# Kernel optimization log

Hardware: AMD Instinct MI355X
Metric: run time of the kernel (lower is better)

The kernel has to match this reference:

```python
import jax, jax.numpy as jnp
import numpy as np

DEG20 = 20.0 * np.pi / 180.0
MIN_PATCH_AREA = 4.0


def _bilinear(p, sy, sx):
    """Bilinear sample [P,P,3] patch at float coords sy,sx of shape [H,W]."""
    P = p.shape[0]
    y0 = jnp.floor(sy)
    x0 = jnp.floor(sx)
    wy = (sy - y0)[..., None]
    wx = (sx - x0)[..., None]
    y0i = jnp.clip(y0, 0, P - 1).astype(jnp.int32)
    y1i = jnp.clip(y0 + 1, 0, P - 1).astype(jnp.int32)
    x0i = jnp.clip(x0, 0, P - 1).astype(jnp.int32)
    x1i = jnp.clip(x0 + 1, 0, P - 1).astype(jnp.int32)
    v00 = p[y0i, x0i]
    v01 = p[y0i, x1i]
    v10 = p[y1i, x0i]
    v11 = p[y1i, x1i]
    return v00 * (1 - wy) * (1 - wx) + v01 * (1 - wy) * wx + v10 * wy * (1 - wx) + v11 * wy * wx


def setup_inputs() -> dict:
    key = jax.random.key(0)
    B, H, W, N, P = 16, 768, 768, 16, 640
    k_img, k_patch, k_ymin, k_xmin, k_h, k_w = jax.random.split(key, 6)
    images = jax.random.uniform(k_img, (B, H, W, 3), jnp.float32, -1.0, 1.0)
    patch = jax.random.uniform(k_patch, (P, P, 3), jnp.float32, -1.0, 1.0)
    ymin = jax.random.uniform(k_ymin, (B, N), jnp.float32, 0.0, 0.55 * H)
    xmin = jax.random.uniform(k_xmin, (B, N), jnp.float32, 0.0, 0.55 * W)
    bh = jax.random.uniform(k_h, (B, N), jnp.float32, 60.0, 0.40 * H)
    bw = jax.random.uniform(k_w, (B, N), jnp.float32, 60.0, 0.40 * W)
    ymax = jnp.minimum(ymin + bh, float(H))
    xmax = jnp.minimum(xmin + bw, float(W))
    boxes = jnp.stack([ymin, xmin, ymax, xmax], axis=-1)  # [B,N,4]
    scale = jnp.float32(0.4)
    return {"images": images, "boxes": boxes, "patch": patch, "scale": scale}


def reference(images, boxes, patch, scale):
    B, H, W, _ = images.shape
    P = patch.shape[0]
    Hf, Wf = jnp.float32(H), jnp.float32(W)
    yy = jnp.arange(H, dtype=jnp.float32)[:, None]  # [H,1]
    xx = jnp.arange(W, dtype=jnp.float32)[None, :]  # [1,W]
    scale_s = jnp.reshape(scale, ())

    def per_image(img, bxs, ikey):
        kw, kb, kboxes = jax.random.split(ikey, 3)
        # random_print_adjust: w*patch + b, clipped
        wmul = 0.5 + 0.1 * jax.random.normal(kw, (1, 1, 3), jnp.float32)
        badd = 0.01 * jax.random.normal(kb, (1, 1, 3), jnp.float32)
        p = jnp.clip(wmul * patch + badd, -1.0, 1.0)
        # brightness matcher: shift patch mean toward image mean
        p = jnp.clip(p + (jnp.mean(img) - jnp.mean(p)), -1.0, 1.0)
        bkeys = jax.random.split(kboxes, bxs.shape[0])

        def step(im, inp):
            box, bk = inp
            k1, k2, k3, k4, k5 = jax.random.split(bk, 5)
            ymin, xmin, ymax, xmax = box[0], box[1], box[2], box[3]
            bh = ymax - ymin
            bw = xmax - xmin
            longer = jnp.maximum(bh, bw)
            psize = jnp.floor(longer * scale_s)            # patch_h == patch_w
            diag = jnp.minimum(jnp.float32(np.sqrt(2.0)) * psize, Wf)
            tol = 0.2
            oy = ymin + bh / 2 + jax.random.uniform(k1, (), jnp.float32, -tol * bh / 2, tol * bh / 2)
            ox = xmin + bw / 2 + jax.random.uniform(k2, (), jnp.float32, -tol * bw / 2, tol * bw / 2)
            y0 = jnp.maximum(oy - diag / 2, 0.0)
            x0 = jnp.maximum(ox - diag / 2, 0.0)
            y0 = jnp.where(y0 + diag > Hf, Hf - diag, y0)
            x0 = jnp.where(x0 + diag > Wf, Wf - diag, x0)
            # TF casts to int32 (truncation; values >= 0 -> floor)
            y0 = jnp.floor(y0)
            x0 = jnp.floor(x0)
            d = jnp.floor(diag)
            ph = psize
            valid = (ph * ph) > MIN_PATCH_AREA
            top = jnp.floor((d - ph) / 2.0)                # pad offset
            angle = jax.random.uniform(k3, (), jnp.float32, -DEG20, DEG20)
            # pixel coords inside the diag x diag patch window
            u = yy - y0                                    # [H,1] -> broadcast [H,W]
            v = xx - x0
            inside = (u >= 0) & (u < d) & (v >= 0) & (v < d)
            c = (d - 1.0) / 2.0
            ca, sa = jnp.cos(angle), jnp.sin(angle)
            iu = c + ca * (u - c) - sa * (v - c)           # inverse rotation about center
            iv = c + sa * (u - c) + ca * (v - c)
            py = iu - top                                  # coords in resized patch
            px = iv - top
            # bilinear resize (half-pixel centers): src = (dst+0.5)*P/ph - 0.5
            sy = (py + 0.5) * (P / ph) - 0.5
            sx = (px + 0.5) * (P / ph) - 0.5
            val = _bilinear(p, sy, sx)                     # [H,W,3]
            noise = jax.random.uniform(k4, (H, W, 3), jnp.float32, -0.01, 0.01)
            delta = jax.random.uniform(k5, (), jnp.float32, -0.3, 0.3)
            val = jnp.clip(val + noise + delta, -1.0, 1.0)
            in_patch = (py >= 0) & (py <= ph - 1) & (px >= 0) & (px <= ph - 1)
            fill = jnp.where(in_patch[..., None], val, -2.0)  # pad/rotate fill = -2
            blended = jnp.clip(jnp.where(fill < -1.0, im, fill), -1.0, 1.0)
            write = inside[..., None] & valid
            return jnp.where(write, blended, im), None

        out, _ = jax.lax.scan(step, img, (bxs, bkeys))
        return out

    ikeys = jax.random.split(jax.random.key(42), B)
    return jax.vmap(per_image)(images, boxes, ikeys)
```

## Files before the change

kernel.cpp:

```cpp
#include <hip/hip_runtime.h>
#include <stdint.h>

#define NIMG 16
#define IMH 768
#define IMW 768
#define NBOX 16
#define PSZ 640
#define IMG_ELEMS (IMH*IMW*3)
#define PATCH_ELEMS (PSZ*PSZ*3)
#define CPBLK 128
#define PATBLK 64
#define PADBLK 64
#define RENDER_BLKS 4096

typedef float f4 __attribute__((ext_vector_type(4)));

__device__ __forceinline__ uint32_t rotl32(uint32_t v, int r){ return (v<<r)|(v>>(32-r)); }

__device__ __forceinline__ void threefry(uint32_t k0, uint32_t k1, uint32_t c0, uint32_t c1,
                                         uint32_t& o0, uint32_t& o1){
  uint32_t ks2 = k0 ^ k1 ^ 0x1BD11BDAu;
  uint32_t x0 = c0 + k0, x1 = c1 + k1;
#define TFR(r) { x0 += x1; x1 = rotl32(x1,(r)); x1 ^= x0; }
  TFR(13) TFR(15) TFR(26) TFR(6)
  x0 += k1;  x1 += ks2 + 1u;
  TFR(17) TFR(29) TFR(16) TFR(24)
  x0 += ks2; x1 += k0 + 2u;
  TFR(13) TFR(15) TFR(26) TFR(6)
  x0 += k0;  x1 += k1 + 3u;
  TFR(17) TFR(29) TFR(16) TFR(24)
  x0 += k1;  x1 += ks2 + 4u;
  TFR(13) TFR(15) TFR(26) TFR(6)
  x0 += ks2; x1 += k0 + 5u;
#undef TFR
  o0 = x0; o1 = x1;
}

__device__ __forceinline__ uint32_t rbits(uint32_t k0, uint32_t k1, uint32_t idx){
  uint32_t a, b; threefry(k0, k1, 0u, idx, a, b); return a ^ b;
}

__device__ __forceinline__ float u01(uint32_t bits){
  return __uint_as_float((bits >> 9) | 0x3f800000u) - 1.0f;
}

__device__ __forceinline__ float juniform(uint32_t k0, uint32_t k1, uint32_t idx, float mn, float mx){
  float u = u01(rbits(k0, k1, idx));
  float span = __fsub_rn(mx, mn);
  return fmaxf(mn, __fadd_rn(__fmul_rn(u, span), mn));
}

__device__ float erfinv32(float x){
  float w = -log1pf(-x*x);
  float p;
  if (w < 5.0f){
    w = w - 2.5f;
    p = 2.81022636e-08f;
    p = fmaf(p,w, 3.43273939e-07f);
    p = fmaf(p,w,-3.5233877e-06f);
    p = fmaf(p,w,-4.39150654e-06f);
    p = fmaf(p,w, 0.00021858087f);
    p = fmaf(p,w,-0.00125372503f);
    p = fmaf(p,w,-0.00417768164f);
    p = fmaf(p,w, 0.246640727f);
    p = fmaf(p,w, 1.50140941f);
  } else {
    w = sqrtf(w) - 3.0f;
    p = -0.000200214257f;
    p = fmaf(p,w, 0.000100950558f);
    p = fmaf(p,w, 0.00134934322f);
    p = fmaf(p,w,-0.00367342844f);
    p = fmaf(p,w, 0.00573950773f);
    p = fmaf(p,w,-0.0076224613f);
    p = fmaf(p,w, 0.00943887047f);
    p = fmaf(p,w, 1.00167406f);
    p = fmaf(p,w, 2.83297682f);
  }
  return p * x;
}

__device__ __forceinline__ void compute_wb(int b, float* rec){
  uint32_t i0,i1; threefry(0u, 42u, 0u, (uint32_t)b, i0, i1);
  uint32_t kw0,kw1; threefry(i0, i1, 0u, 0u, kw0, kw1);
  uint32_t kb0,kb1; threefry(i0, i1, 0u, 1u, kb0, kb1);
  const float lo = -0.99999994f;
  const float span = __fsub_rn(1.0f, lo);
  const float sq2 = 1.4142135623730951f;
  for (int j = 0; j < 3; j++){
    float uw = u01(rbits(kw0, kw1, (uint32_t)j));
    float rw = fmaxf(lo, __fadd_rn(__fmul_rn(uw, span), lo));
    float nw = __fmul_rn(sq2, erfinv32(rw));
    rec[j] = __fadd_rn(0.5f, __fmul_rn(0.1f, nw));
    float ub = u01(rbits(kb0, kb1, (uint32_t)j));
    float rb = fmaxf(lo, __fadd_rn(__fmul_rn(ub, span), lo));
    float nb = __fmul_rn(sq2, erfinv32(rb));
    rec[3+j] = __fmul_rn(0.01f, nb);
  }
  rec[6] = 0.0f; rec[7] = 0.0f;
}

__global__ __launch_bounds__(256) void k_front(const float* __restrict__ img,
                                               const float* __restrict__ patch,
                                               float* __restrict__ out,
                                               double* __restrict__ imgpart,
                                               double* __restrict__ patpart,
                                               f4* __restrict__ pad4, int do_pad){
  if (blockIdx.x < PATBLK){
    __shared__ float wl[NIMG*8];
    if (threadIdx.x < NIMG) compute_wb(threadIdx.x, &wl[threadIdx.x*8]);
    __syncthreads();
    double s[NIMG];
    #pragma unroll
    for (int im = 0; im < NIMG; im++) s[im] = 0.0;
    const f4* p4 = (const f4*)patch;
    const int N4 = PATCH_ELEMS/4;
    for (int i = blockIdx.x*256 + threadIdx.x; i < N4; i += PATBLK*256){
      f4 v = p4[i];
      int c = (i << 2) % 3;
      #pragma unroll
      for (int q = 0; q < 4; q++){
        float pv = v[q];
        #pragma unroll
        for (int im = 0; im < NIMG; im++){
          float t = __fadd_rn(__fmul_rn(wl[im*8 + c], pv), wl[im*8 + 3 + c]);
          t = fminf(fmaxf(t, -1.0f), 1.0f);
          s[im] += (double)t;
        }
        c = (c == 2) ? 0 : c + 1;
      }
    }
    #pragma unroll
    for (int im = 0; im < NIMG; im++)
      for (int o = 32; o > 0; o >>= 1) s[im] += __shfl_down(s[im], o);
    __shared__ double red[4][NIMG];
    if ((threadIdx.x & 63) == 0){
      int w = threadIdx.x >> 6;
      #pragma unroll
      for (int im = 0; im < NIMG; im++) red[w][im] = s[im];
    }
    __syncthreads();
    if (threadIdx.x < NIMG){
      double t = red[0][threadIdx.x] + red[1][threadIdx.x] + red[2][threadIdx.x] + red[3][threadIdx.x];
      patpart[threadIdx.x*PATBLK + blockIdx.x] = t;
    }
  } else if (blockIdx.x < PATBLK + NIMG*CPBLK){
    int bi = blockIdx.x - PATBLK;
    int b = bi >> 7;
    int j = bi & (CPBLK-1);
    const f4* src = (const f4*)(img + (size_t)b * IMG_ELEMS);
    f4* dst = (f4*)(out + (size_t)b * IMG_ELEMS);
    const int N4 = IMG_ELEMS/4;
    f4 fs = {0.0f, 0.0f, 0.0f, 0.0f};
    #pragma unroll 2
    for (int i = j*256 + threadIdx.x; i < N4; i += CPBLK*256){
      f4 v = src[i];
      dst[i] = v;
      fs += v;
    }
    double s = ((double)fs.x + (double)fs.y) + ((double)fs.z + (double)fs.w);
    for (int o = 32; o > 0; o >>= 1) s += __shfl_down(s, o);
    __shared__ double sm[4];
    if ((threadIdx.x & 63) == 0) sm[threadIdx.x >> 6] = s;
    __syncthreads();
    if (threadIdx.x == 0) imgpart[b*CPBLK + j] = sm[0]+sm[1]+sm[2]+sm[3];
  } else {
    if (!do_pad) return;
    int pb = blockIdx.x - (PATBLK + NIMG*CPBLK);
    const f4* src = (const f4*)patch;
    const int NG = PSZ*PSZ/4;
    for (int g = pb*256 + threadIdx.x; g < NG; g += PADBLK*256){
      f4 a = src[g*3+0], b2 = src[g*3+1], c2 = src[g*3+2];
      f4 t0 = {a.x,  a.y,  a.z,  0.0f};
      f4 t1 = {a.w,  b2.x, b2.y, 0.0f};
      f4 t2 = {b2.z, b2.w, c2.x, 0.0f};
      f4 t3 = {c2.y, c2.z, c2.w, 0.0f};
      pad4[g*4+0] = t0; pad4[g*4+1] = t1; pad4[g*4+2] = t2; pad4[g*4+3] = t3;
    }
  }
}

__global__ __launch_bounds__(256) void k_final(const double* __restrict__ imgpart,
                        const double* __restrict__ patpart,
                        float* __restrict__ shift, float* __restrict__ wbg,
                        float* __restrict__ boxp, int* __restrict__ chunkoff,
                        const float* __restrict__ boxes, const float* __restrict__ scale){
  int t = threadIdx.x;
  {
    int im = t >> 4, l = t & 15;
    double si = 0.0, sp = 0.0;
    #pragma unroll
    for (int j = 0; j < CPBLK/16; j++) si += imgpart[im*CPBLK + l + j*16];
    #pragma unroll
    for (int j = 0; j < PATBLK/16; j++) sp += patpart[im*PATBLK + l + j*16];
    #pragma unroll
    for (int o = 8; o > 0; o >>= 1){ si += __shfl_down(si, o); sp += __shfl_down(sp, o); }
    if (l == 0){
      float mi = (float)(si / (double)IMG_ELEMS);
      float mp = (float)(sp / (double)PATCH_ELEMS);
      shift[im] = __fsub_rn(mi, mp);
      compute_wb(im, &wbg[im*8]);
    }
  }

  int nch = 0;
  {
    int b = t / NBOX, i = t % NBOX;
    uint32_t i0,i1;  threefry(0u, 42u, 0u, (uint32_t)b, i0, i1);
    uint32_t kx0,kx1; threefry(i0, i1, 0u, 2u, kx0, kx1);
    uint32_t bk0,bk1; threefry(kx0, kx1, 0u, (uint32_t)i, bk0, bk1);
    uint32_t K1a,K1b,K2a,K2b,K3a,K3b,K4a,K4b,K5a,K5b;
    threefry(bk0,bk1,0u,0u,K1a,K1b);
    threefry(bk0,bk1,0u,1u,K2a,K2b);
    threefry(bk0,bk1,0u,2u,K3a,K3b);
    threefry(bk0,bk1,0u,3u,K4a,K4b);
    threefry(bk0,bk1,0u,4u,K5a,K5b);

    const float* bx = boxes + (size_t)t*4;
    float ymin = bx[0], xmin = bx[1], ymax = bx[2], xmax = bx[3];
    float bh = __fsub_rn(ymax, ymin);
    float bw = __fsub_rn(xmax, xmin);
    float longer = fmaxf(bh, bw);
    float sc = scale[0];
    float psize = floorf(__fmul_rn(longer, sc));
    float diag = fminf(__fmul_rn(1.4142135623730951f, psize), 768.0f);

    float mny = __fdiv_rn(__fmul_rn(-0.2f, bh), 2.0f);
    float mxy = __fdiv_rn(__fmul_rn( 0.2f, bh), 2.0f);
    float r1 = juniform(K1a, K1b, 0u, mny, mxy);
    float oy = __fadd_rn(__fadd_rn(ymin, __fdiv_rn(bh, 2.0f)), r1);
    float mnx = __fdiv_rn(__fmul_rn(-0.2f, bw), 2.0f);
    float mxx = __fdiv_rn(__fmul_rn( 0.2f, bw), 2.0f);
    float r2 = juniform(K2a, K2b, 0u, mnx, mxx);
    float ox = __fadd_rn(__fadd_rn(xmin, __fdiv_rn(bw, 2.0f)), r2);

    float hd = __fdiv_rn(diag, 2.0f);
    float y0 = fmaxf(__fsub_rn(oy, hd), 0.0f);
    float x0 = fmaxf(__fsub_rn(ox, hd), 0.0f);
    if (__fadd_rn(y0, diag) > 768.0f) y0 = __fsub_rn(768.0f, diag);
    if (__fadd_rn(x0, diag) > 768.0f) x0 = __fsub_rn(768.0f, diag);
    y0 = floorf(y0);
    x0 = floorf(x0);
    float d  = floorf(diag);
    float ph = psize;
    float top = floorf(__fdiv_rn(__fsub_rn(d, ph), 2.0f));

    const float A20 = 0.3490658503988659f;
    float ang = juniform(K3a, K3b, 0u, -A20, A20);
    double da = (double)ang;
    float ca = (float)cos(da);
    float sa = (float)sin(da);
    float delta = juniform(K5a, K5b, 0u, -0.3f, 0.3f);
    float valid = (__fmul_rn(ph, ph) > 4.0f) ? 1.0f : 0.0f;
    float cc  = __fdiv_rn(__fsub_rn(d, 1.0f), 2.0f);
    float sres = __fdiv_rn(640.0f, ph);

    float* o = boxp + t*16;
    o[0]=y0; o[1]=x0; o[2]=d; o[3]=ph; o[4]=top; o[5]=cc; o[6]=ca; o[7]=sa;
    o[8]=sres; o[9]=delta;
    o[10]=__uint_as_float(K4a); o[11]=__uint_as_float(K4b);
    o[12]=valid; o[13]=__fsub_rn(ph, 1.0f); o[14]=0.0f; o[15]=0.0f;

    if (valid != 0.0f){
      int di = (int)d;
      nch = (di*di + 255) >> 8;
    }
  }

  __shared__ int scan[256];
  scan[t] = nch; __syncthreads();
  for (int off = 1; off < 256; off <<= 1){
    int v = (t >= off) ? scan[t-off] : 0;
    __syncthreads();
    scan[t] += v;
    __syncthreads();
  }
  if (t == 0) chunkoff[0] = 0;
  chunkoff[t+1] = scan[t];
}

template<int USEPAD>
__global__ __launch_bounds__(256) void k_render3(
    const float* __restrict__ patch, const f4* __restrict__ pad4,
    const float* __restrict__ wbg, const float* __restrict__ shiftg,
    const float* __restrict__ boxp, const int* __restrict__ chunkoff,
    float* __restrict__ out)
{
  __shared__ float sp[256*16];
  __shared__ float wl[NIMG*8];
  __shared__ float shl[NIMG];
  __shared__ int   coff[258];
  for (int i = threadIdx.x; i < 4096; i += 256) sp[i] = boxp[i];
  if (threadIdx.x < NIMG*8) wl[threadIdx.x] = wbg[threadIdx.x];
  if (threadIdx.x < NIMG)   shl[threadIdx.x] = shiftg[threadIdx.x];
  for (int i = threadIdx.x; i < 257; i += 256) coff[i] = chunkoff[i];
  __syncthreads();
  int total = coff[256];

  for (int chunk = blockIdx.x; chunk < total; chunk += RENDER_BLKS){
    int lo = 0, hi = 255;
    #pragma unroll
    for (int it = 0; it < 8; it++){
      int mid = (lo + hi + 1) >> 1;
      if (coff[mid] <= chunk) lo = mid; else hi = mid - 1;
    }
    int s = lo;
    const float* bp = &sp[s*16];
    int d = (int)bp[2];
    int dd = d*d;
    int idx = (chunk - coff[s])*256 + (int)threadIdx.x;
    if (idx >= dd) continue;

    int b = s >> 4, k = s & 15;
    float y0f = bp[0], x0f = bp[1];
    float cc = bp[5], ca = bp[6], sa = bp[7], top = bp[4];
    float ph1 = bp[13], sres = bp[8], delta = bp[9];

    int row = idx / d;
    int col = idx - row*d;
    int y = (int)y0f + row, x = (int)x0f + col;
    float yf = (float)y, xf = (float)x;
    float u = __fsub_rn(yf, y0f), v = __fsub_rn(xf, x0f);
    float um = __fsub_rn(u, cc), vm = __fsub_rn(v, cc);
    float iu = __fsub_rn(__fadd_rn(cc, __fmul_rn(ca, um)), __fmul_rn(sa, vm));
    float iv = __fadd_rn(__fadd_rn(cc, __fmul_rn(sa, um)), __fmul_rn(ca, vm));
    float py = __fsub_rn(iu, top), px = __fsub_rn(iv, top);
    if (!(py >= 0.0f && py <= ph1 && px >= 0.0f && px <= ph1)) continue;

    bool lose = false;
    for (int j = NBOX-1; j > k; --j){
      const float* bq = &sp[(b*NBOX + j)*16];
      if (bq[12] == 0.0f) continue;
      float u2 = __fsub_rn(yf, bq[0]);
      if (!(u2 >= 0.0f && u2 < bq[2])) continue;
      float v2 = __fsub_rn(xf, bq[1]);
      if (!(v2 >= 0.0f && v2 < bq[2])) continue;
      float um2 = __fsub_rn(u2, bq[5]), vm2 = __fsub_rn(v2, bq[5]);
      float iu2 = __fsub_rn(__fadd_rn(bq[5], __fmul_rn(bq[6], um2)), __fmul_rn(bq[7], vm2));
      float iv2 = __fadd_rn(__fadd_rn(bq[5], __fmul_rn(bq[7], um2)), __fmul_rn(bq[6], vm2));
      float py2 = __fsub_rn(iu2, bq[4]), px2 = __fsub_rn(iv2, bq[4]);
      if (py2 >= 0.0f && py2 <= bq[13] && px2 >= 0.0f && px2 <= bq[13]){ lose = true; break; }
    }
    if (lose) continue;

    float sy = __fsub_rn(__fmul_rn(__fadd_rn(py, 0.5f), sres), 0.5f);
    float sx = __fsub_rn(__fmul_rn(__fadd_rn(px, 0.5f), sres), 0.5f);
    float fy = floorf(sy), fx = floorf(sx);
    float wy = __fsub_rn(sy, fy), wx = __fsub_rn(sx, fx);
    int y0t = (int)fminf(fmaxf(fy, 0.0f), 639.0f);
    int y1t = (int)fminf(fmaxf(__fadd_rn(fy, 1.0f), 0.0f), 639.0f);
    int x0t = (int)fminf(fmaxf(fx, 0.0f), 639.0f);
    int x1t = (int)fminf(fmaxf(__fadd_rn(fx, 1.0f), 0.0f), 639.0f);
    float w00 = (1.0f-wy)*(1.0f-wx), w01 = (1.0f-wy)*wx;
    float w10 = wy*(1.0f-wx),        w11 = wy*wx;
    const float* wbb = &wl[b*8];
    float shf = shl[b];
    uint32_t n0 = __float_as_uint(bp[10]);
    uint32_t n1 = __float_as_uint(bp[11]);
    int pix = y*IMW + x;
    size_t base = (size_t)b*IMG_ELEMS + (size_t)pix*3;

    f4 p00, p01, p10, p11;
    int i00, i01, i10, i11;
    if constexpr (USEPAD){
      p00 = pad4[y0t*PSZ + x0t]; p01 = pad4[y0t*PSZ + x1t];
      p10 = pad4[y1t*PSZ + x0t]; p11 = pad4[y1t*PSZ + x1t];
      i00 = i01 = i10 = i11 = 0;
    } else {
      i00 = (y0t*PSZ + x0t)*3; i01 = (y0t*PSZ + x1t)*3;
      i10 = (y1t*PSZ + x0t)*3; i11 = (y1t*PSZ + x1t)*3;
    }
    #pragma unroll
    for (int c = 0; c < 3; c++){
      float wm = wbb[c], bd = wbb[3+c];
      float t00, t01, t10, t11;
      if constexpr (USEPAD){ t00 = p00[c]; t01 = p01[c]; t10 = p10[c]; t11 = p11[c]; }
      else { t00 = patch[i00+c]; t01 = patch[i01+c]; t10 = patch[i10+c]; t11 = patch[i11+c]; }
      float v00 = fminf(fmaxf(__fadd_rn(__fmul_rn(wm, t00), bd), -1.0f), 1.0f);
      v00 = fminf(fmaxf(__fadd_rn(v00, shf), -1.0f), 1.0f);
      float v01 = fminf(fmaxf(__fadd_rn(__fmul_rn(wm, t01), bd), -1.0f), 1.0f);
      v01 = fminf(fmaxf(__fadd_rn(v01, shf), -1.0f), 1.0f);
      float v10 = fminf(fmaxf(__fadd_rn(__fmul_rn(wm, t10), bd), -1.0f), 1.0f);
      v10 = fminf(fmaxf(__fadd_rn(v10, shf), -1.0f), 1.0f);
      float v11 = fminf(fmaxf(__fadd_rn(__fmul_rn(wm, t11), bd), -1.0f), 1.0f);
      v11 = fminf(fmaxf(__fadd_rn(v11, shf), -1.0f), 1.0f);
      float val = v00*w00 + v01*w01 + v10*w10 + v11*w11;
      float un = u01(rbits(n0, n1, (uint32_t)(pix*3 + c)));
      float span = __fsub_rn(0.01f, -0.01f);
      float nz = fmaxf(-0.01f, __fadd_rn(__fmul_rn(un, span), -0.01f));
      val = __fadd_rn(__fadd_rn(val, nz), delta);
      out[base + c] = fminf(fmaxf(val, -1.0f), 1.0f);
    }
  }
}

extern "C" void kernel_launch(void* const* d_in, const int* in_sizes, int n_in,
                              void* d_out, int out_size, void* d_ws, size_t ws_size,
                              hipStream_t stream){
  (void)in_sizes; (void)n_in; (void)out_size;
  const float* images = (const float*)d_in[0];
  const float* boxes  = (const float*)d_in[1];
  const float* patch  = (const float*)d_in[2];
  const float* scale  = (const float*)d_in[3];
  float* out = (float*)d_out;

  char* ws = (char*)d_ws;
  double* imgpart = (double*)(ws);
  double* patpart = (double*)(ws + 16384);
  float*  wb      = (float*)(ws + 24576);
  float*  shift   = (float*)(ws + 25088);
  float*  boxp    = (float*)(ws + 25600);
  int*    chunkoff= (int*)(ws + 41984);
  f4*     pad4    = (f4*)(ws + 65536);

  size_t need = 65536 + (size_t)PSZ*PSZ*16;
  int do_pad = (ws_size >= need) ? 1 : 0;

  int front_blks = PATBLK + NIMG*CPBLK + (do_pad ? PADBLK : 0);
  hipLaunchKernelGGL(k_front,   dim3(front_blks), dim3(256), 0, stream,
                     images, patch, out, imgpart, patpart, pad4, do_pad);
  hipLaunchKernelGGL(k_final,   dim3(1), dim3(256), 0, stream,
                     imgpart, patpart, shift, wb, boxp, chunkoff, boxes, scale);
  if (do_pad)
    hipLaunchKernelGGL(k_render3<1>, dim3(RENDER_BLKS), dim3(256), 0, stream,
                       patch, pad4, wb, shift, boxp, chunkoff, out);
  else
    hipLaunchKernelGGL(k_render3<0>, dim3(RENDER_BLKS), dim3(256), 0, stream,
                       patch, pad4, wb, shift, boxp, chunkoff, out);
}
```

Measured before the change: 139.1 us.

## Fuse image copy into per-pixel render pass using per-row box bitmasks

Drops the separate image copy from the front kernel; it now only computes the image sums. The render kernel now walks every output pixel: it loads the image values, checks per-row bitmasks of covering boxes built in k_final with shared-memory atomics, and composites the topmost patch that covers the pixel. Output is written with nontemporal stores. This removes the write-then-overwrite traffic and the chunk scan with its binary search, but the image is now read twice (once for the sums, once in render) and covered pixels loop over candidate boxes.

```diff
diff --git a/kernel.cpp b/kernel.cpp
--- a/kernel.cpp
+++ b/kernel.cpp
@@ -8,10 +8,10 @@
 #define PSZ 640
 #define IMG_ELEMS (IMH*IMW*3)
 #define PATCH_ELEMS (PSZ*PSZ*3)
-#define CPBLK 128
 #define PATBLK 64
 #define PADBLK 64
-#define RENDER_BLKS 4096
+#define ISUM 64
+#define RBLK_PER_IMG 576
 
 typedef float f4 __attribute__((ext_vector_type(4)));
 
@@ -101,7 +101,6 @@
 
 __global__ __launch_bounds__(256) void k_front(const float* __restrict__ img,
                                                const float* __restrict__ patch,
-                                               float* __restrict__ out,
                                                double* __restrict__ imgpart,
                                                double* __restrict__ patpart,
                                                f4* __restrict__ pad4, int do_pad){
@@ -143,29 +142,9 @@
       double t = red[0][threadIdx.x] + red[1][threadIdx.x] + red[2][threadIdx.x] + red[3][threadIdx.x];
       patpart[threadIdx.x*PATBLK + blockIdx.x] = t;
     }
-  } else if (blockIdx.x < PATBLK + NIMG*CPBLK){
-    int bi = blockIdx.x - PATBLK;
-    int b = bi >> 7;
-    int j = bi & (CPBLK-1);
-    const f4* src = (const f4*)(img + (size_t)b * IMG_ELEMS);
-    f4* dst = (f4*)(out + (size_t)b * IMG_ELEMS);
-    const int N4 = IMG_ELEMS/4;
-    f4 fs = {0.0f, 0.0f, 0.0f, 0.0f};
-    #pragma unroll 2
-    for (int i = j*256 + threadIdx.x; i < N4; i += CPBLK*256){
-      f4 v = src[i];
-      dst[i] = v;
-      fs += v;
-    }
-    double s = ((double)fs.x + (double)fs.y) + ((double)fs.z + (double)fs.w);
-    for (int o = 32; o > 0; o >>= 1) s += __shfl_down(s, o);
-    __shared__ double sm[4];
-    if ((threadIdx.x & 63) == 0) sm[threadIdx.x >> 6] = s;
-    __syncthreads();
-    if (threadIdx.x == 0) imgpart[b*CPBLK + j] = sm[0]+sm[1]+sm[2]+sm[3];
-  } else {
+  } else if (blockIdx.x < PATBLK + PADBLK){
     if (!do_pad) return;
-    int pb = blockIdx.x - (PATBLK + NIMG*CPBLK);
+    int pb = blockIdx.x - PATBLK;
     const f4* src = (const f4*)patch;
     const int NG = PSZ*PSZ/4;
     for (int g = pb*256 + threadIdx.x; g < NG; g += PADBLK*256){
@@ -176,20 +155,40 @@
       f4 t3 = {c2.y, c2.z, c2.w, 0.0f};
       pad4[g*4+0] = t0; pad4[g*4+1] = t1; pad4[g*4+2] = t2; pad4[g*4+3] = t3;
     }
+  } else {
+    int bi = blockIdx.x - (PATBLK + PADBLK);
+    int b = bi >> 6;
+    int j = bi & (ISUM-1);
+    const f4* src = (const f4*)(img + (size_t)b * IMG_ELEMS);
+    const int N4 = IMG_ELEMS/4;
+    f4 fs = {0.0f, 0.0f, 0.0f, 0.0f};
+    for (int i = j*256 + threadIdx.x; i < N4; i += ISUM*256){
+      f4 v = src[i];
+      fs += v;
+    }
+    double s = ((double)fs.x + (double)fs.y) + ((double)fs.z + (double)fs.w);
+    for (int o = 32; o > 0; o >>= 1) s += __shfl_down(s, o);
+    __shared__ double sm[4];
+    if ((threadIdx.x & 63) == 0) sm[threadIdx.x >> 6] = s;
+    __syncthreads();
+    if (threadIdx.x == 0) imgpart[b*ISUM + j] = sm[0]+sm[1]+sm[2]+sm[3];
   }
 }
 
 __global__ __launch_bounds__(256) void k_final(const double* __restrict__ imgpart,
                         const double* __restrict__ patpart,
                         float* __restrict__ shift, float* __restrict__ wbg,
-                        float* __restrict__ boxp, int* __restrict__ chunkoff,
+                        float* __restrict__ boxp, uint32_t* __restrict__ masks,
                         const float* __restrict__ boxes, const float* __restrict__ scale){
   int t = threadIdx.x;
+  __shared__ uint32_t rm[NIMG*IMH];
+  for (int i = t; i < NIMG*IMH; i += 256) rm[i] = 0u;
+
   {
     int im = t >> 4, l = t & 15;
     double si = 0.0, sp = 0.0;
     #pragma unroll
-    for (int j = 0; j < CPBLK/16; j++) si += imgpart[im*CPBLK + l + j*16];
+    for (int j = 0; j < ISUM/16; j++) si += imgpart[im*ISUM + l + j*16];
     #pragma unroll
     for (int j = 0; j < PATBLK/16; j++) sp += patpart[im*PATBLK + l + j*16];
     #pragma unroll
@@ -201,8 +200,8 @@
       compute_wb(im, &wbg[im*8]);
     }
   }
-
-  int nch = 0;
+  __syncthreads();
+
   {
     int b = t / NBOX, i = t % NBOX;
     uint32_t i0,i1;  threefry(0u, 42u, 0u, (uint32_t)b, i0, i1);
@@ -261,136 +260,125 @@
     o[12]=valid; o[13]=__fsub_rn(ph, 1.0f); o[14]=0.0f; o[15]=0.0f;
 
     if (valid != 0.0f){
-      int di = (int)d;
-      nch = (di*di + 255) >> 8;
-    }
-  }
-
-  __shared__ int scan[256];
-  scan[t] = nch; __syncthreads();
-  for (int off = 1; off < 256; off <<= 1){
-    int v = (t >= off) ? scan[t-off] : 0;
-    __syncthreads();
-    scan[t] += v;
-    __syncthreads();
-  }
-  if (t == 0) chunkoff[0] = 0;
-  chunkoff[t+1] = scan[t];
+      int y0i = (int)y0, di = (int)d;
+      uint32_t bit = 1u << i;
+      for (int y = y0i; y < y0i + di; y++)
+        atomicOr(&rm[b*IMH + y], bit);
+    }
+  }
+  __syncthreads();
+  for (int i = t; i < NIMG*IMH; i += 256) masks[i] = rm[i];
 }
 
 template<int USEPAD>
-__global__ __launch_bounds__(256) void k_render3(
-    const float* __restrict__ patch, const f4* __restrict__ pad4,
-    const float* __restrict__ wbg, const float* __restrict__ shiftg,
-    const float* __restrict__ boxp, const int* __restrict__ chunkoff,
-    float* __restrict__ out)
+__global__ __launch_bounds__(256) void k_render4(
+    const float* __restrict__ img, const float* __restrict__ patch,
+    const f4* __restrict__ pad4, const float* __restrict__ wbg,
+    const float* __restrict__ shiftg, const float* __restrict__ boxp,
+    const uint32_t* __restrict__ masks, float* __restrict__ out)
 {
-  __shared__ float sp[256*16];
-  __shared__ float wl[NIMG*8];
-  __shared__ float shl[NIMG];
-  __shared__ int   coff[258];
-  for (int i = threadIdx.x; i < 4096; i += 256) sp[i] = boxp[i];
-  if (threadIdx.x < NIMG*8) wl[threadIdx.x] = wbg[threadIdx.x];
-  if (threadIdx.x < NIMG)   shl[threadIdx.x] = shiftg[threadIdx.x];
-  for (int i = threadIdx.x; i < 257; i += 256) coff[i] = chunkoff[i];
+  int b   = blockIdx.x / RBLK_PER_IMG;
+  int blk = blockIdx.x - b*RBLK_PER_IMG;
+
+  __shared__ float sp[NBOX*16];
+  __shared__ float wl[8];
+  __shared__ float shl;
+  sp[threadIdx.x] = boxp[b*NBOX*16 + threadIdx.x];
+  if (threadIdx.x < 8) wl[threadIdx.x] = wbg[b*8 + threadIdx.x];
+  if (threadIdx.x == 0) shl = shiftg[b];
   __syncthreads();
-  int total = coff[256];
-
-  for (int chunk = blockIdx.x; chunk < total; chunk += RENDER_BLKS){
-    int lo = 0, hi = 255;
-    #pragma unroll
-    for (int it = 0; it < 8; it++){
-      int mid = (lo + hi + 1) >> 1;
-      if (coff[mid] <= chunk) lo = mid; else hi = mid - 1;
-    }
-    int s = lo;
-    const float* bp = &sp[s*16];
-    int d = (int)bp[2];
-    int dd = d*d;
-    int idx = (chunk - coff[s])*256 + (int)threadIdx.x;
-    if (idx >= dd) continue;
-
-    int b = s >> 4, k = s & 15;
-    float y0f = bp[0], x0f = bp[1];
-    float cc = bp[5], ca = bp[6], sa = bp[7], top = bp[4];
-    float ph1 = bp[13], sres = bp[8], delta = bp[9];
-
-    int row = idx / d;
-    int col = idx - row*d;
-    int y = (int)y0f + row, x = (int)x0f + col;
-    float yf = (float)y, xf = (float)x;
-    float u = __fsub_rn(yf, y0f), v = __fsub_rn(xf, x0f);
-    float um = __fsub_rn(u, cc), vm = __fsub_rn(v, cc);
-    float iu = __fsub_rn(__fadd_rn(cc, __fmul_rn(ca, um)), __fmul_rn(sa, vm));
-    float iv = __fadd_rn(__fadd_rn(cc, __fmul_rn(sa, um)), __fmul_rn(ca, vm));
-    float py = __fsub_rn(iu, top), px = __fsub_rn(iv, top);
-    if (!(py >= 0.0f && py <= ph1 && px >= 0.0f && px <= ph1)) continue;
-
-    bool lose = false;
-    for (int j = NBOX-1; j > k; --j){
-      const float* bq = &sp[(b*NBOX + j)*16];
-      if (bq[12] == 0.0f) continue;
-      float u2 = __fsub_rn(yf, bq[0]);
-      if (!(u2 >= 0.0f && u2 < bq[2])) continue;
-      float v2 = __fsub_rn(xf, bq[1]);
-      if (!(v2 >= 0.0f && v2 < bq[2])) continue;
-      float um2 = __fsub_rn(u2, bq[5]), vm2 = __fsub_rn(v2, bq[5]);
-      float iu2 = __fsub_rn(__fadd_rn(bq[5], __fmul_rn(bq[6], um2)), __fmul_rn(bq[7], vm2));
-      float iv2 = __fadd_rn(__fadd_rn(bq[5], __fmul_rn(bq[7], um2)), __fmul_rn(bq[6], vm2));
-      float py2 = __fsub_rn(iu2, bq[4]), px2 = __fsub_rn(iv2, bq[4]);
-      if (py2 >= 0.0f && py2 <= bq[13] && px2 >= 0.0f && px2 <= bq[13]){ lose = true; break; }
-    }
-    if (lose) continue;
-
-    float sy = __fsub_rn(__fmul_rn(__fadd_rn(py, 0.5f), sres), 0.5f);
-    float sx = __fsub_rn(__fmul_rn(__fadd_rn(px, 0.5f), sres), 0.5f);
-    float fy = floorf(sy), fx = floorf(sx);
-    float wy = __fsub_rn(sy, fy), wx = __fsub_rn(sx, fx);
-    int y0t = (int)fminf(fmaxf(fy, 0.0f), 639.0f);
-    int y1t = (int)fminf(fmaxf(__fadd_rn(fy, 1.0f), 0.0f), 639.0f);
-    int x0t = (int)fminf(fmaxf(fx, 0.0f), 639.0f);
-    int x1t = (int)fminf(fmaxf(__fadd_rn(fx, 1.0f), 0.0f), 639.0f);
-    float w00 = (1.0f-wy)*(1.0f-wx), w01 = (1.0f-wy)*wx;
-    float w10 = wy*(1.0f-wx),        w11 = wy*wx;
-    const float* wbb = &wl[b*8];
-    float shf = shl[b];
-    uint32_t n0 = __float_as_uint(bp[10]);
-    uint32_t n1 = __float_as_uint(bp[11]);
-    int pix = y*IMW + x;
-    size_t base = (size_t)b*IMG_ELEMS + (size_t)pix*3;
-
-    f4 p00, p01, p10, p11;
-    int i00, i01, i10, i11;
-    if constexpr (USEPAD){
-      p00 = pad4[y0t*PSZ + x0t]; p01 = pad4[y0t*PSZ + x1t];
-      p10 = pad4[y1t*PSZ + x0t]; p11 = pad4[y1t*PSZ + x1t];
-      i00 = i01 = i10 = i11 = 0;
-    } else {
-      i00 = (y0t*PSZ + x0t)*3; i01 = (y0t*PSZ + x1t)*3;
-      i10 = (y1t*PSZ + x0t)*3; i11 = (y1t*PSZ + x1t)*3;
-    }
-    #pragma unroll
-    for (int c = 0; c < 3; c++){
-      float wm = wbb[c], bd = wbb[3+c];
-      float t00, t01, t10, t11;
-      if constexpr (USEPAD){ t00 = p00[c]; t01 = p01[c]; t10 = p10[c]; t11 = p11[c]; }
-      else { t00 = patch[i00+c]; t01 = patch[i01+c]; t10 = patch[i10+c]; t11 = patch[i11+c]; }
-      float v00 = fminf(fmaxf(__fadd_rn(__fmul_rn(wm, t00), bd), -1.0f), 1.0f);
-      v00 = fminf(fmaxf(__fadd_rn(v00, shf), -1.0f), 1.0f);
-      float v01 = fminf(fmaxf(__fadd_rn(__fmul_rn(wm, t01), bd), -1.0f), 1.0f);
-      v01 = fminf(fmaxf(__fadd_rn(v01, shf), -1.0f), 1.0f);
-      float v10 = fminf(fmaxf(__fadd_rn(__fmul_rn(wm, t10), bd), -1.0f), 1.0f);
-      v10 = fminf(fmaxf(__fadd_rn(v10, shf), -1.0f), 1.0f);
-      float v11 = fminf(fmaxf(__fadd_rn(__fmul_rn(wm, t11), bd), -1.0f), 1.0f);
-      v11 = fminf(fmaxf(__fadd_rn(v11, shf), -1.0f), 1.0f);
-      float val = v00*w00 + v01*w01 + v10*w10 + v11*w11;
-      float un = u01(rbits(n0, n1, (uint32_t)(pix*3 + c)));
-      float span = __fsub_rn(0.01f, -0.01f);
-      float nz = fmaxf(-0.01f, __fadd_rn(__fmul_rn(un, span), -0.01f));
-      val = __fadd_rn(__fadd_rn(val, nz), delta);
-      out[base + c] = fminf(fmaxf(val, -1.0f), 1.0f);
-    }
-  }
+
+  int pixbase = blk*1024 + (int)threadIdx.x*4;
+  int y = pixbase / IMW;
+  int xb = pixbase - y*IMW;
+  float yf = (float)y;
+
+  const f4* src = (const f4*)(img + (size_t)b*IMG_ELEMS);
+  f4* dst = (f4*)(out + (size_t)b*IMG_ELEMS);
+  int vbase = blk*768 + (int)threadIdx.x*3;
+  f4 A = src[vbase+0], Bv = src[vbase+1], Cv = src[vbase+2];
+  float arr[12];
+  arr[0]=A.x; arr[1]=A.y; arr[2]=A.z; arr[3]=A.w;
+  arr[4]=Bv.x; arr[5]=Bv.y; arr[6]=Bv.z; arr[7]=Bv.w;
+  arr[8]=Cv.x; arr[9]=Cv.y; arr[10]=Cv.z; arr[11]=Cv.w;
+
+  uint32_t m0 = masks[b*IMH + y];
+
+  if (m0){
+    #pragma unroll
+    for (int g = 0; g < 4; g++){
+      float xf = (float)(xb + g);
+      uint32_t m = m0;
+      bool done = false;
+      while (m && !done){
+        int j = 31 - __clz(m);
+        m &= ~(1u << j);
+        const float* bq = &sp[j*16];
+        float v2 = __fsub_rn(xf, bq[1]);
+        if (!(v2 >= 0.0f && v2 < bq[2])) continue;
+        float u2 = __fsub_rn(yf, bq[0]);
+        float cc2 = bq[5];
+        float um2 = __fsub_rn(u2, cc2), vm2 = __fsub_rn(v2, cc2);
+        float iu2 = __fsub_rn(__fadd_rn(cc2, __fmul_rn(bq[6], um2)), __fmul_rn(bq[7], vm2));
+        float iv2 = __fadd_rn(__fadd_rn(cc2, __fmul_rn(bq[7], um2)), __fmul_rn(bq[6], vm2));
+        float py = __fsub_rn(iu2, bq[4]), px = __fsub_rn(iv2, bq[4]);
+        if (!(py >= 0.0f && py <= bq[13] && px >= 0.0f && px <= bq[13])) continue;
+        done = true;
+        float sres = bq[8], delta = bq[9];
+        uint32_t n0 = __float_as_uint(bq[10]);
+        uint32_t n1 = __float_as_uint(bq[11]);
+        float sy = __fsub_rn(__fmul_rn(__fadd_rn(py, 0.5f), sres), 0.5f);
+        float sx = __fsub_rn(__fmul_rn(__fadd_rn(px, 0.5f), sres), 0.5f);
+        float fy = floorf(sy), fx = floorf(sx);
+        float wy = __fsub_rn(sy, fy), wx = __fsub_rn(sx, fx);
+        int y0t = (int)fminf(fmaxf(fy, 0.0f), 639.0f);
+        int y1t = (int)fminf(fmaxf(__fadd_rn(fy, 1.0f), 0.0f), 639.0f);
+        int x0t = (int)fminf(fmaxf(fx, 0.0f), 639.0f);
+        int x1t = (int)fminf(fmaxf(__fadd_rn(fx, 1.0f), 0.0f), 639.0f);
+        float w00 = (1.0f-wy)*(1.0f-wx), w01 = (1.0f-wy)*wx;
+        float w10 = wy*(1.0f-wx),        w11 = wy*wx;
+        f4 p00, p01, p10, p11;
+        int i00, i01, i10, i11;
+        if constexpr (USEPAD){
+          p00 = pad4[y0t*PSZ + x0t]; p01 = pad4[y0t*PSZ + x1t];
+          p10 = pad4[y1t*PSZ + x0t]; p11 = pad4[y1t*PSZ + x1t];
+          i00 = i01 = i10 = i11 = 0;
+        } else {
+          i00 = (y0t*PSZ + x0t)*3; i01 = (y0t*PSZ + x1t)*3;
+          i10 = (y1t*PSZ + x0t)*3; i11 = (y1t*PSZ + x1t)*3;
+        }
+        int pix = pixbase + g;
+        #pragma unroll
+        for (int c = 0; c < 3; c++){
+          float wm = wl[c], bd = wl[3+c];
+          float t00, t01, t10, t11;
+          if constexpr (USEPAD){ t00 = p00[c]; t01 = p01[c]; t10 = p10[c]; t11 = p11[c]; }
+          else { t00 = patch[i00+c]; t01 = patch[i01+c]; t10 = patch[i10+c]; t11 = patch[i11+c]; }
+          float v00 = fminf(fmaxf(__fadd_rn(__fmul_rn(wm, t00), bd), -1.0f), 1.0f);
+          v00 = fminf(fmaxf(__fadd_rn(v00, shl), -1.0f), 1.0f);
+          float v01 = fminf(fmaxf(__fadd_rn(__fmul_rn(wm, t01), bd), -1.0f), 1.0f);
+          v01 = fminf(fmaxf(__fadd_rn(v01, shl), -1.0f), 1.0f);
+          float v10 = fminf(fmaxf(__fadd_rn(__fmul_rn(wm, t10), bd), -1.0f), 1.0f);
+          v10 = fminf(fmaxf(__fadd_rn(v10, shl), -1.0f), 1.0f);
+          float v11 = fminf(fmaxf(__fadd_rn(__fmul_rn(wm, t11), bd), -1.0f), 1.0f);
+          v11 = fminf(fmaxf(__fadd_rn(v11, shl), -1.0f), 1.0f);
+          float val = v00*w00 + v01*w01 + v10*w10 + v11*w11;
+          float un = u01(rbits(n0, n1, (uint32_t)(pix*3 + c)));
+          float span = __fsub_rn(0.01f, -0.01f);
+          float nz = fmaxf(-0.01f, __fadd_rn(__fmul_rn(un, span), -0.01f));
+          val = __fadd_rn(__fadd_rn(val, nz), delta);
+          arr[g*3 + c] = fminf(fmaxf(val, -1.0f), 1.0f);
+        }
+      }
+    }
+  }
+
+  f4 o0 = {arr[0], arr[1], arr[2], arr[3]};
+  f4 o1 = {arr[4], arr[5], arr[6], arr[7]};
+  f4 o2 = {arr[8], arr[9], arr[10], arr[11]};
+  __builtin_nontemporal_store(o0, dst + vbase + 0);
+  __builtin_nontemporal_store(o1, dst + vbase + 1);
+  __builtin_nontemporal_store(o2, dst + vbase + 2);
 }
 
 extern "C" void kernel_launch(void* const* d_in, const int* in_sizes, int n_in,
@@ -404,26 +392,25 @@
   float* out = (float*)d_out;
 
   char* ws = (char*)d_ws;
-  double* imgpart = (double*)(ws);
-  double* patpart = (double*)(ws + 16384);
-  float*  wb      = (float*)(ws + 24576);
-  float*  shift   = (float*)(ws + 25088);
-  float*  boxp    = (float*)(ws + 25600);
-  int*    chunkoff= (int*)(ws + 41984);
-  f4*     pad4    = (f4*)(ws + 65536);
-
-  size_t need = 65536 + (size_t)PSZ*PSZ*16;
+  double*   imgpart = (double*)(ws);
+  double*   patpart = (double*)(ws + 8192);
+  float*    wb      = (float*)(ws + 16384);
+  float*    shift   = (float*)(ws + 16896);
+  float*    boxp    = (float*)(ws + 17408);
+  uint32_t* masks   = (uint32_t*)(ws + 33792);
+  f4*       pad4    = (f4*)(ws + 98304);
+
+  size_t need = 98304 + (size_t)PSZ*PSZ*16;
   int do_pad = (ws_size >= need) ? 1 : 0;
 
-  int front_blks = PATBLK + NIMG*CPBLK + (do_pad ? PADBLK : 0);
-  hipLaunchKernelGGL(k_front,   dim3(front_blks), dim3(256), 0, stream,
-                     images, patch, out, imgpart, patpart, pad4, do_pad);
-  hipLaunchKernelGGL(k_final,   dim3(1), dim3(256), 0, stream,
-                     imgpart, patpart, shift, wb, boxp, chunkoff, boxes, scale);
+  hipLaunchKernelGGL(k_front, dim3(PATBLK + PADBLK + NIMG*ISUM), dim3(256), 0, stream,
+                     images, patch, imgpart, patpart, pad4, do_pad);
+  hipLaunchKernelGGL(k_final, dim3(1), dim3(256), 0, stream,
+                     imgpart, patpart, shift, wb, boxp, masks, boxes, scale);
   if (do_pad)
-    hipLaunchKernelGGL(k_render3<1>, dim3(RENDER_BLKS), dim3(256), 0, stream,
-                       patch, pad4, wb, shift, boxp, chunkoff, out);
+    hipLaunchKernelGGL(k_render4<1>, dim3(NIMG*RBLK_PER_IMG), dim3(256), 0, stream,
+                       images, patch, pad4, wb, shift, boxp, masks, out);
   else
-    hipLaunchKernelGGL(k_render3<0>, dim3(RENDER_BLKS), dim3(256), 0, stream,
-                       patch, pad4, wb, shift, boxp, chunkoff, out);
-}
+    hipLaunchKernelGGL(k_render4<0>, dim3(NIMG*RBLK_PER_IMG), dim3(256), 0, stream,
+                       images, patch, pad4, wb, shift, boxp, masks, out);
+}
```

After: 186.2 us. 33.9% more time.

## Unroll image copy with nontemporal ops and precompute box-overlap masks

Applied to the files above, without the earlier changes.

The image copy-and-sum blocks now use 64 blocks per image with a fully unrolled loop of 27 nontemporal vector loads and stores per thread. This exposes more memory parallelism and keeps the streaming copy from polluting the cache. The pad blocks move ahead of the copy blocks so they are scheduled first. The finalize kernel precomputes a per-box bitmask of later boxes whose square bounding regions overlap, and the render kernel walks only those boxes when checking occlusion instead of scanning every later box. The cost is a hardcoded trip count tied to the image size, plus a little extra work in the single-block finalize kernel.

```diff
diff --git a/kernel.cpp b/kernel.cpp
--- a/kernel.cpp
+++ b/kernel.cpp
@@ -8,9 +8,9 @@
 #define PSZ 640
 #define IMG_ELEMS (IMH*IMW*3)
 #define PATCH_ELEMS (PSZ*PSZ*3)
-#define CPBLK 128
 #define PATBLK 64
 #define PADBLK 64
+#define ISUM 64
 #define RENDER_BLKS 4096
 
 typedef float f4 __attribute__((ext_vector_type(4)));
@@ -143,29 +143,9 @@
       double t = red[0][threadIdx.x] + red[1][threadIdx.x] + red[2][threadIdx.x] + red[3][threadIdx.x];
       patpart[threadIdx.x*PATBLK + blockIdx.x] = t;
     }
-  } else if (blockIdx.x < PATBLK + NIMG*CPBLK){
-    int bi = blockIdx.x - PATBLK;
-    int b = bi >> 7;
-    int j = bi & (CPBLK-1);
-    const f4* src = (const f4*)(img + (size_t)b * IMG_ELEMS);
-    f4* dst = (f4*)(out + (size_t)b * IMG_ELEMS);
-    const int N4 = IMG_ELEMS/4;
-    f4 fs = {0.0f, 0.0f, 0.0f, 0.0f};
-    #pragma unroll 2
-    for (int i = j*256 + threadIdx.x; i < N4; i += CPBLK*256){
-      f4 v = src[i];
-      dst[i] = v;
-      fs += v;
-    }
-    double s = ((double)fs.x + (double)fs.y) + ((double)fs.z + (double)fs.w);
-    for (int o = 32; o > 0; o >>= 1) s += __shfl_down(s, o);
-    __shared__ double sm[4];
-    if ((threadIdx.x & 63) == 0) sm[threadIdx.x >> 6] = s;
-    __syncthreads();
-    if (threadIdx.x == 0) imgpart[b*CPBLK + j] = sm[0]+sm[1]+sm[2]+sm[3];
-  } else {
+  } else if (blockIdx.x < PATBLK + PADBLK){
     if (!do_pad) return;
-    int pb = blockIdx.x - (PATBLK + NIMG*CPBLK);
+    int pb = blockIdx.x - PATBLK;
     const f4* src = (const f4*)patch;
     const int NG = PSZ*PSZ/4;
     for (int g = pb*256 + threadIdx.x; g < NG; g += PADBLK*256){
@@ -176,6 +156,52 @@
       f4 t3 = {c2.y, c2.z, c2.w, 0.0f};
       pad4[g*4+0] = t0; pad4[g*4+1] = t1; pad4[g*4+2] = t2; pad4[g*4+3] = t3;
     }
+  } else {
+    int bi = blockIdx.x - (PATBLK + PADBLK);
+    int b = bi >> 6;
+    int j = bi & (ISUM-1);
+    const f4* src = (const f4*)(img + (size_t)b * IMG_ELEMS);
+    f4* dst = (f4*)(out + (size_t)b * IMG_ELEMS);
+    const int STRIDE = ISUM*256;
+    int i = j*256 + (int)threadIdx.x;
+    f4 acc = {0.0f, 0.0f, 0.0f, 0.0f};
+    #pragma unroll 1
+    for (int g = 0; g < 3; ++g){
+      f4 v0 = __builtin_nontemporal_load(src + i + 0*STRIDE);
+      f4 v1 = __builtin_nontemporal_load(src + i + 1*STRIDE);
+      f4 v2 = __builtin_nontemporal_load(src + i + 2*STRIDE);
+      f4 v3 = __builtin_nontemporal_load(src + i + 3*STRIDE);
+      f4 v4 = __builtin_nontemporal_load(src + i + 4*STRIDE);
+      f4 v5 = __builtin_nontemporal_load(src + i + 5*STRIDE);
+      f4 v6 = __builtin_nontemporal_load(src + i + 6*STRIDE);
+      f4 v7 = __builtin_nontemporal_load(src + i + 7*STRIDE);
+      __builtin_nontemporal_store(v0, dst + i + 0*STRIDE);
+      __builtin_nontemporal_store(v1, dst + i + 1*STRIDE);
+      __builtin_nontemporal_store(v2, dst + i + 2*STRIDE);
+      __builtin_nontemporal_store(v3, dst + i + 3*STRIDE);
+      __builtin_nontemporal_store(v4, dst + i + 4*STRIDE);
+      __builtin_nontemporal_store(v5, dst + i + 5*STRIDE);
+      __builtin_nontemporal_store(v6, dst + i + 6*STRIDE);
+      __builtin_nontemporal_store(v7, dst + i + 7*STRIDE);
+      acc += v0; acc += v1; acc += v2; acc += v3;
+      acc += v4; acc += v5; acc += v6; acc += v7;
+      i += 8*STRIDE;
+    }
+    {
+      f4 v0 = __builtin_nontemporal_load(src + i + 0*STRIDE);
+      f4 v1 = __builtin_nontemporal_load(src + i + 1*STRIDE);
+      f4 v2 = __builtin_nontemporal_load(src + i + 2*STRIDE);
+      __builtin_nontemporal_store(v0, dst + i + 0*STRIDE);
+      __builtin_nontemporal_store(v1, dst + i + 1*STRIDE);
+      __builtin_nontemporal_store(v2, dst + i + 2*STRIDE);
+      acc += v0; acc += v1; acc += v2;
+    }
+    double s = ((double)acc.x + (double)acc.y) + ((double)acc.z + (double)acc.w);
+    for (int o = 32; o > 0; o >>= 1) s += __shfl_down(s, o);
+    __shared__ double sm[4];
+    if ((threadIdx.x & 63) == 0) sm[threadIdx.x >> 6] = s;
+    __syncthreads();
+    if (threadIdx.x == 0) imgpart[b*ISUM + j] = sm[0]+sm[1]+sm[2]+sm[3];
   }
 }
 
@@ -189,7 +215,7 @@
     int im = t >> 4, l = t & 15;
     double si = 0.0, sp = 0.0;
     #pragma unroll
-    for (int j = 0; j < CPBLK/16; j++) si += imgpart[im*CPBLK + l + j*16];
+    for (int j = 0; j < ISUM/16; j++) si += imgpart[im*ISUM + l + j*16];
     #pragma unroll
     for (int j = 0; j < PATBLK/16; j++) sp += patpart[im*PATBLK + l + j*16];
     #pragma unroll
@@ -202,7 +228,9 @@
     }
   }
 
+  __shared__ float sy0[256], sx0[256], sd[256], sv[256];
   int nch = 0;
+  float* o = boxp + t*16;
   {
     int b = t / NBOX, i = t % NBOX;
     uint32_t i0,i1;  threefry(0u, 42u, 0u, (uint32_t)b, i0, i1);
@@ -254,16 +282,28 @@
     float cc  = __fdiv_rn(__fsub_rn(d, 1.0f), 2.0f);
     float sres = __fdiv_rn(640.0f, ph);
 
-    float* o = boxp + t*16;
     o[0]=y0; o[1]=x0; o[2]=d; o[3]=ph; o[4]=top; o[5]=cc; o[6]=ca; o[7]=sa;
     o[8]=sres; o[9]=delta;
     o[10]=__uint_as_float(K4a); o[11]=__uint_as_float(K4b);
-    o[12]=valid; o[13]=__fsub_rn(ph, 1.0f); o[14]=0.0f; o[15]=0.0f;
-
+    o[12]=valid; o[13]=__fsub_rn(ph, 1.0f); o[15]=0.0f;
+
+    sy0[t]=y0; sx0[t]=x0; sd[t]=d; sv[t]=valid;
     if (valid != 0.0f){
       int di = (int)d;
       nch = (di*di + 255) >> 8;
     }
+  }
+  __syncthreads();
+  {
+    int i = t & 15, base = t & ~15;
+    uint32_t om = 0u;
+    for (int j = i+1; j < NBOX; j++){
+      int tj = base + j;
+      if (sv[tj] == 0.0f) continue;
+      if (sy0[t] < sy0[tj]+sd[tj] && sy0[tj] < sy0[t]+sd[t] &&
+          sx0[t] < sx0[tj]+sd[tj] && sx0[tj] < sx0[t]+sd[t]) om |= (1u << j);
+    }
+    o[14] = __uint_as_float(om);
   }
 
   __shared__ int scan[256];
@@ -310,7 +350,7 @@
     int idx = (chunk - coff[s])*256 + (int)threadIdx.x;
     if (idx >= dd) continue;
 
-    int b = s >> 4, k = s & 15;
+    int b = s >> 4;
     float y0f = bp[0], x0f = bp[1];
     float cc = bp[5], ca = bp[6], sa = bp[7], top = bp[4];
     float ph1 = bp[13], sres = bp[8], delta = bp[9];
@@ -326,10 +366,12 @@
     float py = __fsub_rn(iu, top), px = __fsub_rn(iv, top);
     if (!(py >= 0.0f && py <= ph1 && px >= 0.0f && px <= ph1)) continue;
 
+    uint32_t m = __float_as_uint(bp[14]);
     bool lose = false;
-    for (int j = NBOX-1; j > k; --j){
-      const float* bq = &sp[(b*NBOX + j)*16];
-      if (bq[12] == 0.0f) continue;
+    while (m){
+      int j = 31 - __clz(m);
+      m &= ~(1u << j);
+      const float* bq = &sp[((s & ~15) + j)*16];
       float u2 = __fsub_rn(yf, bq[0]);
       if (!(u2 >= 0.0f && u2 < bq[2])) continue;
       float v2 = __fsub_rn(xf, bq[1]);
@@ -405,20 +447,19 @@
 
   char* ws = (char*)d_ws;
   double* imgpart = (double*)(ws);
-  double* patpart = (double*)(ws + 16384);
-  float*  wb      = (float*)(ws + 24576);
-  float*  shift   = (float*)(ws + 25088);
-  float*  boxp    = (float*)(ws + 25600);
-  int*    chunkoff= (int*)(ws + 41984);
+  double* patpart = (double*)(ws + 8192);
+  float*  wb      = (float*)(ws + 16384);
+  float*  shift   = (float*)(ws + 16896);
+  float*  boxp    = (float*)(ws + 17408);
+  int*    chunkoff= (int*)(ws + 33792);
   f4*     pad4    = (f4*)(ws + 65536);
 
   size_t need = 65536 + (size_t)PSZ*PSZ*16;
   int do_pad = (ws_size >= need) ? 1 : 0;
 
-  int front_blks = PATBLK + NIMG*CPBLK + (do_pad ? PADBLK : 0);
-  hipLaunchKernelGGL(k_front,   dim3(front_blks), dim3(256), 0, stream,
+  hipLaunchKernelGGL(k_front, dim3(PATBLK + PADBLK + NIMG*ISUM), dim3(256), 0, stream,
                      images, patch, out, imgpart, patpart, pad4, do_pad);
-  hipLaunchKernelGGL(k_final,   dim3(1), dim3(256), 0, stream,
+  hipLaunchKernelGGL(k_final, dim3(1), dim3(256), 0, stream,
                      imgpart, patpart, shift, wb, boxp, chunkoff, boxes, scale);
   if (do_pad)
     hipLaunchKernelGGL(k_render3<1>, dim3(RENDER_BLKS), dim3(256), 0, stream,
```

Measured after the change: 114.5 us. 1.21x faster.
